# Optimization experiments

Measured on AMD Instinct MI355X. Metric: run time of the kernel, lower is better.

The kernel has to match this reference:

```python
import jax, jax.numpy as jnp
import numpy as np
from jax import lax

LAMBDA_SEQ_LEN = 4096
INPUT_SEQ_LEN = 2048
TD_EXT_STEPS = 2048
EPS = 1e-8


def setup_inputs() -> dict:
    key = jax.random.key(0)
    k1, = jax.random.split(key, 1)
    # raw (pre-tanh) parameters; tanh(raw) should land in (0, 1) like atanh-initialized values
    raw_lambd = jax.random.uniform(k1, (LAMBDA_SEQ_LEN,), dtype=jnp.float32, minval=0.5, maxval=2.0)
    raw_gamma = jnp.arctanh(jnp.float32(0.99))
    return {
        "raw_gamma": raw_gamma,
        "raw_lambd": raw_lambd,
        "input_seq_len": INPUT_SEQ_LEN,
        "td_extension_steps": TD_EXT_STEPS,
    }


def reference(raw_gamma, raw_lambd, input_seq_len, td_extension_steps):
    total_seq_len = input_seq_len + td_extension_steps
    gamma = jnp.maximum(jnp.tanh(raw_gamma), EPS)            # scalar
    lambdas = jnp.maximum(jnp.tanh(raw_lambd), EPS)          # [L]
    input_lambd = lambdas[-input_seq_len:]                   # [input_seq_len]
    td_lambd = lambdas[-td_extension_steps:]                 # [td_extension_steps]
    lambd = jnp.concatenate([input_lambd, td_lambd], axis=0)  # [total_seq_len]

    # Reversed linear recurrence: v_t = gamma * (1 - l_t + l_t * v_{t+1}), v_T = 1
    def step(v, l):
        v_new = gamma * (1.0 - l + l * v)
        w = jnp.maximum(1.0 - v_new, EPS)
        return v_new, w

    _, raw_w = lax.scan(step, jnp.float32(1.0), lambd, reverse=True)  # [total_seq_len]

    raw_w = raw_w[None, :, None]                              # [1, T, 1]
    normalized = raw_w / jnp.maximum(raw_w.mean(), EPS)
    # module stores normalized[:, :input_seq_len] and normalized[:, input_seq_len:];
    # return the full normalized weights (concatenation of both buffers)
    return normalized
```

## Files before the change

kernel.cpp:

```cpp
#include <hip/hip_runtime.h>
#include <math.h>

#define EPS 1e-8f

__global__ __launch_bounds__(256) void GammaLambdaLearner_kernel(
    const float* __restrict__ raw_gamma,
    const float* __restrict__ raw_lambd,
    float* __restrict__ out)
{
    constexpr int N    = 4096;
    constexpr int HALF = 2048;
    constexpr int T    = 256;
    constexpr int C    = N / T;

    __shared__ float s_lam[HALF];
    __shared__ float sA[T];
    __shared__ float sB[T];
    __shared__ float s_carry[T];
    __shared__ float s_red[T / 64];
    __shared__ float s_inv;

    const int t = threadIdx.x;
    const float gamma = fmaxf(tanhf(raw_gamma[0]), EPS);

    for (int i = t; i < HALF; i += T)
        s_lam[i] = fmaxf(tanhf(raw_lambd[HALF + i]), EPS);
    __syncthreads();

    const int base = t * C;
    float l[C];
    #pragma unroll
    for (int j = 0; j < C; ++j)
        l[j] = s_lam[(base + j) & (HALF - 1)];

    float A = 0.f, B = 1.f;
    #pragma unroll
    for (int j = C - 1; j >= 0; --j) {
        const float a = gamma * (1.f - l[j]);
        const float b = gamma * l[j];
        A = fmaf(b, A, a);
        B = b * B;
    }
    sA[t] = A;
    sB[t] = B;
    __syncthreads();

    if (t == 0) {
        float v = 1.f;
        for (int k = T - 1; k >= 0; --k) {
            s_carry[k] = v;
            v = fmaf(sB[k], v, sA[k]);
        }
    }
    __syncthreads();

    float w[C];
    float v = s_carry[t];
    float lsum = 0.f;
    #pragma unroll
    for (int j = C - 1; j >= 0; --j) {
        const float a = gamma * (1.f - l[j]);
        v = fmaf(gamma * l[j], v, a);
        w[j] = fmaxf(1.f - v, EPS);
        lsum += w[j];
    }

    #pragma unroll
    for (int off = 32; off > 0; off >>= 1)
        lsum += __shfl_down(lsum, off, 64);
    if ((t & 63) == 0) s_red[t >> 6] = lsum;
    __syncthreads();
    if (t == 0) {
        const float s = s_red[0] + s_red[1] + s_red[2] + s_red[3];
        const float mean = s * (1.f / (float)N);
        s_inv = 1.f / fmaxf(mean, EPS);
    }
    __syncthreads();

    const float inv = s_inv;
    #pragma unroll
    for (int j = 0; j < C; ++j)
        out[base + j] = w[j] * inv;
}

extern "C" void kernel_launch(void* const* d_in, const int* in_sizes, int n_in,
                              void* d_out, int out_size, void* d_ws, size_t ws_size,
                              hipStream_t stream) {
    const float* raw_gamma = (const float*)d_in[0];
    const float* raw_lambd = (const float*)d_in[1];
    float* out = (float*)d_out;
    GammaLambdaLearner_kernel<<<1, 256, 0, stream>>>(raw_gamma, raw_lambd, out);
}
```

Baseline: 68.29 us.

## Replace serial carry scan with wave-shuffle parallel scan, vectorize IO, fast tanh

Replaces the single-thread serial loop over 256 chunk carries with a parallel affine-composition scan, done with wave shuffles inside each wave and then across the four waves through shared memory. It also drops the shared staging of lambdas: each thread loads its 16 raw values with float4 reads and applies a fast exp/rcp-based tanh itself. Outputs are written as float4. The fast tanh and the reordered composition change rounding slightly, and fast_tanh can return NaN for large inputs where exp overflows.

After: 59.36 us. 13.1% less time.

```diff
diff --git a/kernel.cpp b/kernel.cpp
--- a/kernel.cpp
+++ b/kernel.cpp
@@ -2,6 +2,11 @@
 #include <math.h>
 
 #define EPS 1e-8f
+
+__device__ __forceinline__ float fast_tanh(float x) {
+    const float e = __expf(2.0f * x);
+    return (e - 1.0f) * __builtin_amdgcn_rcpf(e + 1.0f);
+}
 
 __global__ __launch_bounds__(256) void GammaLambdaLearner_kernel(
     const float* __restrict__ raw_gamma,
@@ -13,74 +18,86 @@
     constexpr int T    = 256;
     constexpr int C    = N / T;
 
-    __shared__ float s_lam[HALF];
-    __shared__ float sA[T];
-    __shared__ float sB[T];
-    __shared__ float s_carry[T];
-    __shared__ float s_red[T / 64];
+    __shared__ float sWA[4], sWB[4];
+    __shared__ float sV[T + 1];
+    __shared__ float s_red[4];
     __shared__ float s_inv;
 
-    const int t = threadIdx.x;
-    const float gamma = fmaxf(tanhf(raw_gamma[0]), EPS);
-
-    for (int i = t; i < HALF; i += T)
-        s_lam[i] = fmaxf(tanhf(raw_lambd[HALF + i]), EPS);
-    __syncthreads();
+    const int t    = threadIdx.x;
+    const int lane = t & 63;
+    const int wave = t >> 6;
+    const float gamma = fmaxf(fast_tanh(raw_gamma[0]), EPS);
 
     const int base = t * C;
-    float l[C];
+    const float4* src =
+        (const float4*)(raw_lambd + HALF + (base & (HALF - 1)));
+    float4 q0 = src[0], q1 = src[1], q2 = src[2], q3 = src[3];
+    float l[C] = {q0.x, q0.y, q0.z, q0.w, q1.x, q1.y, q1.z, q1.w,
+                  q2.x, q2.y, q2.z, q2.w, q3.x, q3.y, q3.z, q3.w};
     #pragma unroll
     for (int j = 0; j < C; ++j)
-        l[j] = s_lam[(base + j) & (HALF - 1)];
+        l[j] = fmaxf(fast_tanh(l[j]), EPS);
 
     float A = 0.f, B = 1.f;
     #pragma unroll
     for (int j = C - 1; j >= 0; --j) {
-        const float a = gamma * (1.f - l[j]);
         const float b = gamma * l[j];
+        const float a = gamma - b;
         A = fmaf(b, A, a);
         B = b * B;
     }
-    sA[t] = A;
-    sB[t] = B;
+
+    #pragma unroll
+    for (int d = 1; d < 64; d <<= 1) {
+        float An = __shfl_down(A, d, 64);
+        float Bn = __shfl_down(B, d, 64);
+        const bool valid = (lane + d) < 64;
+        An = valid ? An : 0.f;
+        Bn = valid ? Bn : 1.f;
+        A = fmaf(B, An, A);
+        B = B * Bn;
+    }
+    if (lane == 0) { sWA[wave] = A; sWB[wave] = B; }
     __syncthreads();
 
-    if (t == 0) {
-        float v = 1.f;
-        for (int k = T - 1; k >= 0; --k) {
-            s_carry[k] = v;
-            v = fmaf(sB[k], v, sA[k]);
-        }
+    for (int w = wave + 1; w < 4; ++w) {
+        const float An = sWA[w], Bn = sWB[w];
+        A = fmaf(B, An, A);
+        B = B * Bn;
     }
+
+    sV[t] = A + B;
+    if (t == 0) sV[T] = 1.f;
     __syncthreads();
 
-    float w[C];
-    float v = s_carry[t];
+    float w_[C];
+    float v    = sV[t + 1];
     float lsum = 0.f;
     #pragma unroll
     for (int j = C - 1; j >= 0; --j) {
-        const float a = gamma * (1.f - l[j]);
-        v = fmaf(gamma * l[j], v, a);
-        w[j] = fmaxf(1.f - v, EPS);
-        lsum += w[j];
+        const float b = gamma * l[j];
+        v = fmaf(b, v, gamma - b);
+        w_[j] = fmaxf(1.f - v, EPS);
+        lsum += w_[j];
     }
 
     #pragma unroll
     for (int off = 32; off > 0; off >>= 1)
         lsum += __shfl_down(lsum, off, 64);
-    if ((t & 63) == 0) s_red[t >> 6] = lsum;
+    if (lane == 0) s_red[wave] = lsum;
     __syncthreads();
     if (t == 0) {
         const float s = s_red[0] + s_red[1] + s_red[2] + s_red[3];
-        const float mean = s * (1.f / (float)N);
-        s_inv = 1.f / fmaxf(mean, EPS);
+        s_inv = 1.f / fmaxf(s * (1.f / (float)N), EPS);
     }
     __syncthreads();
 
     const float inv = s_inv;
-    #pragma unroll
-    for (int j = 0; j < C; ++j)
-        out[base + j] = w[j] * inv;
+    float4* dst = (float4*)(out + base);
+    dst[0] = make_float4(w_[0] * inv, w_[1] * inv, w_[2]  * inv, w_[3]  * inv);
+    dst[1] = make_float4(w_[4] * inv, w_[5] * inv, w_[6]  * inv, w_[7]  * inv);
+    dst[2] = make_float4(w_[8] * inv, w_[9] * inv, w_[10] * inv, w_[11] * inv);
+    dst[3] = make_float4(w_[12]* inv, w_[13]* inv, w_[14] * inv, w_[15] * inv);
 }
 
 extern "C" void kernel_launch(void* const* d_in, const int* in_sizes, int n_in,
```
